# Performance work log

Measured on AMD Instinct MI355X. Metric: run time of the kernel, lower is better.

Reference implementation:

```python
import jax, jax.numpy as jnp
import numpy as np

N = 50000
E = 600000
H = 128   # hidden_channels (input to decoder)
O = 128   # output_channels (LSTM hidden size)
S = 8     # seq_len


def setup_inputs() -> dict:
    key = jax.random.key(0)
    ks = jax.random.split(key, 10)
    x = jax.random.normal(ks[0], (N, H), dtype=jnp.float32)
    c = jax.random.normal(ks[1], (N, H), dtype=jnp.float32)
    edge_index = jax.random.randint(ks[2], (2, E), 0, N, dtype=jnp.int64)
    # GCNConv weights (PyG: out = norm_agg(x @ W) + b)
    sc = lambda fan_in: 1.0 / np.sqrt(fan_in)
    Wh = jax.random.uniform(ks[3], (H, O), jnp.float32, -sc(H), sc(H))
    bh = jnp.zeros((O,), jnp.float32)
    Wc = jax.random.uniform(ks[4], (H, O), jnp.float32, -sc(H), sc(H))
    bc = jnp.zeros((O,), jnp.float32)
    # per-timestep cell convs: GCNConv(H + O, 4*O)
    Wcell = jax.random.uniform(ks[5], (S, H + O, 4 * O), jnp.float32, -sc(H + O), sc(H + O))
    bcell = jnp.zeros((S, 4 * O), jnp.float32)
    return {"x": x, "c": c, "edge_index": edge_index,
            "Wh": Wh, "bh": bh, "Wc": Wc, "bc": bc,
            "Wcell": Wcell, "bcell": bcell}


def _gcn(feat, W, b, src, dst, dinv):
    # PyG GCNConv with default add_self_loops=True, edge_weight=None:
    # out = D^{-1/2}(A+I)D^{-1/2} (feat @ W) + b
    xw = feat @ W                                   # [N, C_out]
    norm = (dinv[src] * dinv[dst])[:, None]         # [E, 1]
    agg = jax.ops.segment_sum(xw[src] * norm, dst, num_segments=N)
    agg = agg + (dinv * dinv)[:, None] * xw         # self-loop term
    return agg + b


def reference(x, c, edge_index, Wh, bh, Wc, bc, Wcell, bcell):
    src = edge_index[0]
    dst = edge_index[1]
    # degree (with self-loops, unit edge weights); computed on target index
    deg = jax.ops.segment_sum(jnp.ones((E,), jnp.float32), dst, num_segments=N) + 1.0
    dinv = 1.0 / jnp.sqrt(deg)

    h_cur = _gcn(x, Wh, bh, src, dst, dinv)
    c_cur = _gcn(c, Wc, bc, src, dst, dinv)

    def step(carry, params):
        h, cs = carry
        W, b = params
        combined = jnp.concatenate([x, h], axis=1)          # [N, H+O]
        cc = _gcn(combined, W, b, src, dst, dinv)           # [N, 4O]
        cc_f, cc_i, cc_o, cc_g = jnp.split(cc, 4, axis=1)
        f = jax.nn.sigmoid(cc_f)
        i = jax.nn.sigmoid(cc_i)
        o = jax.nn.sigmoid(cc_o)
        g = jnp.tanh(cc_g)
        c_next = f * cs + i * g
        h_next = o * jnp.tanh(c_next)
        return (h_next, c_next), h_next

    (h_fin, c_fin), hs = jax.lax.scan(step, (h_cur, c_cur), (Wcell, bcell))
    return hs, (h_fin, c_fin)  # hs: [S, N, O]
```

## Files before the change

### kernel.cpp

```cpp
#include <hip/hip_runtime.h>
#include <hip/hip_bf16.h>
#include <hip/hip_fp16.h>
#include <cstddef>


#define TPB 256

typedef __attribute__((ext_vector_type(8))) short bf16x8;
typedef __attribute__((ext_vector_type(4))) float f32x4;

__device__ __forceinline__ float sigf(float x) {
    return 1.0f / (1.0f + __expf(-x));
}
__device__ __forceinline__ float tanhfast(float x) {
    return 1.0f - 2.0f / (__expf(2.0f * x) + 1.0f);
}


__global__ void k_hist(const int* __restrict__ dst, int* __restrict__ counts, int E) {
    int stride = gridDim.x * TPB;
    for (int e = blockIdx.x * TPB + threadIdx.x; e < E; e += stride)
        atomicAdd(&counts[dst[e]], 1);
}

__global__ void k_scan_block(const int* __restrict__ counts, int* __restrict__ offsets,
                             int* __restrict__ sums, int N) {
    __shared__ int s[TPB];
    int tid = threadIdx.x;
    int gid = blockIdx.x * TPB + tid;
    int v = (gid < N) ? counts[gid] : 0;
    s[tid] = v;
    __syncthreads();
    for (int d = 1; d < TPB; d <<= 1) {
        int t = (tid >= d) ? s[tid - d] : 0;
        __syncthreads();
        s[tid] += t;
        __syncthreads();
    }
    if (gid < N) offsets[gid] = s[tid] - v;
    if (tid == TPB - 1) sums[blockIdx.x] = s[tid];
}

__global__ void k_scan_tops(int* __restrict__ sums, int nb) {
    __shared__ int s[TPB];
    int tid = threadIdx.x;
    int v = (tid < nb) ? sums[tid] : 0;
    s[tid] = v;
    __syncthreads();
    for (int d = 1; d < TPB; d <<= 1) {
        int t = (tid >= d) ? s[tid - d] : 0;
        __syncthreads();
        s[tid] += t;
        __syncthreads();
    }
    if (tid < nb) sums[tid] = s[tid] - v;
}

__global__ void k_scan_finish(const int* __restrict__ counts, int* __restrict__ offsets,
                              const int* __restrict__ sums, int* __restrict__ cursor,
                              float* __restrict__ dinv, int N, int E) {
    int gid = blockIdx.x * TPB + threadIdx.x;
    if (gid < N) {
        int off = offsets[gid] + sums[blockIdx.x];
        offsets[gid] = off;
        cursor[gid]  = off;
        dinv[gid]    = rsqrtf((float)(counts[gid] + 1));
    }
    if (gid == 0) offsets[N] = E;
}

__global__ void k_csr_scatter(const int* __restrict__ src, const int* __restrict__ dst,
                              const float* __restrict__ dinv, int* __restrict__ cursor,
                              int2* __restrict__ csr_sw, int E) {
    int stride = gridDim.x * TPB;
    for (int e = blockIdx.x * TPB + threadIdx.x; e < E; e += stride) {
        int d = dst[e], s = src[e];
        int pos = atomicAdd(&cursor[d], 1);
        int2 r;
        r.x = s;
        r.y = __float_as_int(dinv[s] * dinv[d]);
        csr_sw[pos] = r;
    }
}


__global__ void k_f32tof16_2(const float* __restrict__ a, const float* __restrict__ b,
                             __half* __restrict__ oa, __half* __restrict__ ob, int n4) {
    int stride = gridDim.x * TPB;
    for (int i = blockIdx.x * TPB + threadIdx.x; i < n4; i += stride) {
        float4 va = ((const float4*)a)[i];
        float4 vb = ((const float4*)b)[i];
        ((__half2*)oa)[2 * i]     = __floats2half2_rn(va.x, va.y);
        ((__half2*)oa)[2 * i + 1] = __floats2half2_rn(va.z, va.w);
        ((__half2*)ob)[2 * i]     = __floats2half2_rn(vb.x, vb.y);
        ((__half2*)ob)[2 * i + 1] = __floats2half2_rn(vb.z, vb.w);
    }
}


union HU { f32x4 v; __half2 h[4]; };

__global__ __launch_bounds__(TPB) void k_aggregate_h(
        const __half* __restrict__ feat, __hip_bfloat16* __restrict__ agg,
        const int* __restrict__ offsets, const int2* __restrict__ sw,
        const float* __restrict__ dinv, int N) {
    int wid = blockIdx.x * 4 + (threadIdx.x >> 6);
    int nw = gridDim.x * 4;
    int lane = threadIdx.x & 63;
    int g = lane >> 4, t = lane & 15;
    const f32x4* f4 = (const f32x4*)feat;

    for (int n0 = wid * 2; n0 < N; n0 += nw * 2) {
        int n1 = n0 + 1;
        bool has1 = (n1 < N);
        int b0 = offsets[n0], e0 = offsets[n0 + 1];
        int b1 = has1 ? offsets[n1] : 0;
        int e1 = has1 ? offsets[n1 + 1] : 0;
        int s0 = (e0 > b0) ? e0 - 1 : 0;
        int s1 = (e1 > b1) ? e1 - 1 : 0;
        int it0 = (e0 - b0 + 3) >> 2;
        int it1 = (e1 - b1 + 3) >> 2;
        int nit = it0 > it1 ? it0 : it1;

        float acc0[8], acc1[8];
        #pragma unroll
        for (int j = 0; j < 8; ++j) { acc0[j] = 0.f; acc1[j] = 0.f; }

        for (int i = 0; i < nit; ++i) {
            int kk0 = b0 + 4 * i + g;
            int kc0 = (kk0 < e0) ? kk0 : s0;
            int kk1 = b1 + 4 * i + g;
            int kc1 = (kk1 < e1) ? kk1 : s1;
            int2 v0 = sw[kc0];
            int2 v1 = sw[kc1];
            float w0 = (kk0 < e0) ? __int_as_float(v0.y) : 0.f;
            float w1 = (kk1 < e1) ? __int_as_float(v1.y) : 0.f;
            HU u0, u1;
            u0.v = f4[(size_t)v0.x * 16 + t];
            u1.v = f4[(size_t)v1.x * 16 + t];
            #pragma unroll
            for (int j = 0; j < 4; ++j) {
                float2 p0 = __half22float2(u0.h[j]);
                float2 p1 = __half22float2(u1.h[j]);
                acc0[2 * j]     = fmaf(w0, p0.x, acc0[2 * j]);
                acc0[2 * j + 1] = fmaf(w0, p0.y, acc0[2 * j + 1]);
                acc1[2 * j]     = fmaf(w1, p1.x, acc1[2 * j]);
                acc1[2 * j + 1] = fmaf(w1, p1.y, acc1[2 * j + 1]);
            }
        }
        #pragma unroll
        for (int j = 0; j < 8; ++j) {
            acc0[j] += __shfl_xor(acc0[j], 16);
            acc0[j] += __shfl_xor(acc0[j], 32);
            acc1[j] += __shfl_xor(acc1[j], 16);
            acc1[j] += __shfl_xor(acc1[j], 32);
        }
        if (g == 0) {
            {
                float di = dinv[n0];
                float w0 = di * di;
                HU u;
                u.v = f4[(size_t)n0 * 16 + t];
                union { f32x4 v; __hip_bfloat162 b2[4]; } o;
                #pragma unroll
                for (int j = 0; j < 4; ++j) {
                    float2 vv = __half22float2(u.h[j]);
                    o.b2[j].x = __float2bfloat16(fmaf(w0, vv.x, acc0[2 * j]));
                    o.b2[j].y = __float2bfloat16(fmaf(w0, vv.y, acc0[2 * j + 1]));
                }
                *(f32x4*)(agg + (size_t)n0 * 128 + t * 8) = o.v;
            }
            if (has1) {
                float di = dinv[n1];
                float w0 = di * di;
                HU u;
                u.v = f4[(size_t)n1 * 16 + t];
                union { f32x4 v; __hip_bfloat162 b2[4]; } o;
                #pragma unroll
                for (int j = 0; j < 4; ++j) {
                    float2 vv = __half22float2(u.h[j]);
                    o.b2[j].x = __float2bfloat16(fmaf(w0, vv.x, acc1[2 * j]));
                    o.b2[j].y = __float2bfloat16(fmaf(w0, vv.y, acc1[2 * j + 1]));
                }
                *(f32x4*)(agg + (size_t)n1 * 128 + t * 8) = o.v;
            }
        }
    }
}

__global__ __launch_bounds__(TPB) void k_aggregate_h2(
        const __half* __restrict__ fa, const __half* __restrict__ fb,
        __hip_bfloat16* __restrict__ aggA, __hip_bfloat16* __restrict__ aggB,
        const int* __restrict__ offsets, const int2* __restrict__ sw,
        const float* __restrict__ dinv, int N) {
    int wgid = blockIdx.x * 4 + (threadIdx.x >> 6);
    int nwaves = gridDim.x * 4;
    int lane = threadIdx.x & 63;
    int g = lane >> 4, t = lane & 15;
    const f32x4* fa4 = (const f32x4*)fa;
    const f32x4* fb4 = (const f32x4*)fb;

    for (int node = wgid; node < N; node += nwaves) {
        float accA[8], accB[8];
        #pragma unroll
        for (int j = 0; j < 8; ++j) { accA[j] = 0.f; accB[j] = 0.f; }

        int b = offsets[node], e = offsets[node + 1];
        for (int k = b; k < e; k += 4) {
            int kk = k + g;
            int kkc = (kk < e) ? kk : (e - 1);
            int2 sv = sw[kkc];
            float w = (kk < e) ? __int_as_float(sv.y) : 0.f;
            size_t ri = (size_t)sv.x * 16 + t;
            HU ua, ub;
            ua.v = fa4[ri];
            ub.v = fb4[ri];
            #pragma unroll
            for (int j = 0; j < 4; ++j) {
                float2 va = __half22float2(ua.h[j]);
                float2 vb = __half22float2(ub.h[j]);
                accA[2 * j]     = fmaf(w, va.x, accA[2 * j]);
                accA[2 * j + 1] = fmaf(w, va.y, accA[2 * j + 1]);
                accB[2 * j]     = fmaf(w, vb.x, accB[2 * j]);
                accB[2 * j + 1] = fmaf(w, vb.y, accB[2 * j + 1]);
            }
        }
        #pragma unroll
        for (int j = 0; j < 8; ++j) {
            accA[j] += __shfl_xor(accA[j], 16);
            accA[j] += __shfl_xor(accA[j], 32);
            accB[j] += __shfl_xor(accB[j], 16);
            accB[j] += __shfl_xor(accB[j], 32);
        }
        if (g == 0) {
            float di = dinv[node];
            float w0 = di * di;
            size_t ri = (size_t)node * 16 + t;
            HU ua, ub;
            ua.v = fa4[ri];
            ub.v = fb4[ri];
            union { f32x4 v; __hip_bfloat162 b2[4]; } oa, ob;
            #pragma unroll
            for (int j = 0; j < 4; ++j) {
                float2 va = __half22float2(ua.h[j]);
                float2 vb = __half22float2(ub.h[j]);
                oa.b2[j].x = __float2bfloat16(fmaf(w0, va.x, accA[2 * j]));
                oa.b2[j].y = __float2bfloat16(fmaf(w0, va.y, accA[2 * j + 1]));
                ob.b2[j].x = __float2bfloat16(fmaf(w0, vb.x, accB[2 * j]));
                ob.b2[j].y = __float2bfloat16(fmaf(w0, vb.y, accB[2 * j + 1]));
            }
            *(f32x4*)(aggA + (size_t)node * 128 + t * 8) = oa.v;
            *(f32x4*)(aggB + (size_t)node * 128 + t * 8) = ob.v;
        }
    }
}


__global__ void k_pack_w128_2(const float* __restrict__ Wh, const float* __restrict__ Wc,
                              __hip_bfloat16* __restrict__ WhP, __hip_bfloat16* __restrict__ WcP) {
    int gid = blockIdx.x * TPB + threadIdx.x;
    if (gid >= 32768) return;
    const float* W = (gid < 16384) ? Wh : Wc;
    __hip_bfloat16* Wp = (gid < 16384) ? WhP : WcP;
    int idx = gid & 16383;
    int j = idx & 7, lane = (idx >> 3) & 63, pblk = (idx >> 9) & 7, ks = idx >> 12;
    int k = ks * 32 + (lane >> 4) * 8 + j;
    int col = pblk * 16 + (lane & 15);
    Wp[idx] = __float2bfloat16(W[k * 128 + col]);
}

__global__ void k_pack_wcell(const float* __restrict__ W, __hip_bfloat16* __restrict__ Wp, int S) {
    int total = S * 131072;
    int stride = gridDim.x * TPB;
    for (int idx = blockIdx.x * TPB + threadIdx.x; idx < total; idx += stride) {
        int j = idx & 7, lane = (idx >> 3) & 63, pblk = (idx >> 9) & 31;
        int ks = (idx >> 14) & 7, s = idx >> 17;
        int p = pblk * 16 + (lane & 15);
        int jcol = p >> 2, gate = p & 3;
        int k = ks * 32 + (lane >> 4) * 8 + j;
        Wp[idx] = __float2bfloat16(W[(size_t)s * 131072 + k * 512 + gate * 128 + jcol]);
    }
}


__global__ __launch_bounds__(TPB) void k_gemm_t(
        const __hip_bfloat16* __restrict__ Ap,
        const __hip_bfloat16* __restrict__ featb,
        const float* __restrict__ bias, float* __restrict__ Cout,
        __half* __restrict__ outh, int N) {
    __shared__ __align__(16) short Bs[128 * 40];
    int tid = threadIdx.x;
    int wave = tid >> 6, lane = tid & 63;
    int w_p = wave >> 1, w_n = wave & 1;
    int n0 = blockIdx.x * 128;
    int quad = lane >> 4, m16 = lane & 15;
    f32x4 zero = {0.f, 0.f, 0.f, 0.f};
    f32x4 acc[4][4];
    #pragma unroll
    for (int t = 0; t < 4; ++t)
        #pragma unroll
        for (int g = 0; g < 4; ++g) acc[t][g] = zero;

    for (int ks = 0; ks < 4; ++ks) {
        int kbase = ks * 32;
        __syncthreads();
        #pragma unroll
        for (int it = 0; it < 2; ++it) {
            int lin = it * TPB + tid;
            int row = lin >> 2, seg = lin & 3;
            int node = n0 + row;
            f32x4 v = zero;
            if (node < N) v = *(const f32x4*)(featb + (size_t)node * 128 + kbase + seg * 8);
            *(f32x4*)&Bs[row * 40 + seg * 8] = v;
        }
        __syncthreads();
        bf16x8 a[4], b[4];
        #pragma unroll
        for (int t = 0; t < 4; ++t)
            a[t] = *(const bf16x8*)(Ap + (((size_t)ks * 8 + w_p * 4 + t) * 64 + lane) * 8);
        #pragma unroll
        for (int g = 0; g < 4; ++g)
            b[g] = *(const bf16x8*)&Bs[(w_n * 64 + g * 16 + m16) * 40 + quad * 8];
        #pragma unroll
        for (int t = 0; t < 4; ++t)
            #pragma unroll
            for (int g = 0; g < 4; ++g)
                acc[t][g] = __builtin_amdgcn_mfma_f32_16x16x32_bf16(a[t], b[g], acc[t][g], 0, 0, 0);
    }
    #pragma unroll
    for (int t = 0; t < 4; ++t) {
        int p = w_p * 64 + t * 16 + quad * 4;
        f32x4 bv = *(const f32x4*)(bias + p);
        #pragma unroll
        for (int g = 0; g < 4; ++g) {
            int nd = n0 + w_n * 64 + g * 16 + m16;
            if (nd < N) {
                f32x4 o = acc[t][g] + bv;
                if (Cout) *(f32x4*)(Cout + (size_t)nd * 128 + p) = o;
                if (outh) {
                    __half2 lo = __floats2half2_rn(o.x, o.y);
                    __half2 hi = __floats2half2_rn(o.z, o.w);
                    __half2* hp = (__half2*)(outh + (size_t)nd * 128 + p);
                    hp[0] = lo;
                    hp[1] = hi;
                }
            }
        }
    }
}


__global__ __launch_bounds__(TPB) void k_cell_t(
        const __hip_bfloat16* __restrict__ Ap,
        const __hip_bfloat16* __restrict__ axb, const __hip_bfloat16* __restrict__ ahb,
        const float* __restrict__ bias,
        float* __restrict__ cbuf, float* __restrict__ hout,
        __half* __restrict__ houth,
        float* __restrict__ hfin, int N) {
    __shared__ __align__(16) short Bs[8][128 * 40];
    int tid = threadIdx.x;
    int wave = tid >> 6, lane = tid & 63;
    int w_p = wave >> 1, w_n = wave & 1;
    int n0 = blockIdx.x * 128;
    int quad = lane >> 4, m16 = lane & 15;
    f32x4 zero = {0.f, 0.f, 0.f, 0.f};

    #pragma unroll
    for (int it = 0; it < 16; ++it) {
        int ks = it >> 1;
        int lin = ((it & 1) << 8) + tid;
        int row = lin >> 2, seg = lin & 3;
        const __hip_bfloat16* fsrc = (ks < 4) ? axb : ahb;
        int node = n0 + row;
        f32x4 v = zero;
        if (node < N) v = *(const f32x4*)(fsrc + (size_t)node * 128 + (ks & 3) * 32 + seg * 8);
        *(f32x4*)&Bs[ks][row * 40 + seg * 8] = v;
    }
    __syncthreads();

    for (int p0i = 0; p0i < 4; ++p0i) {
        f32x4 acc[4][4];
        #pragma unroll
        for (int t = 0; t < 4; ++t)
            #pragma unroll
            for (int g = 0; g < 4; ++g) acc[t][g] = zero;

        #pragma unroll
        for (int ks = 0; ks < 8; ++ks) {
            bf16x8 a[4], b[4];
            #pragma unroll
            for (int t = 0; t < 4; ++t)
                a[t] = *(const bf16x8*)(Ap + (((size_t)ks * 32 + p0i * 8 + w_p * 4 + t) * 64 + lane) * 8);
            #pragma unroll
            for (int g = 0; g < 4; ++g)
                b[g] = *(const bf16x8*)&Bs[ks][(w_n * 64 + g * 16 + m16) * 40 + quad * 8];
            #pragma unroll
            for (int t = 0; t < 4; ++t)
                #pragma unroll
                for (int g = 0; g < 4; ++g)
                    acc[t][g] = __builtin_amdgcn_mfma_f32_16x16x32_bf16(a[t], b[g], acc[t][g], 0, 0, 0);
        }

        #pragma unroll
        for (int t = 0; t < 4; ++t) {
            int p = p0i * 128 + w_p * 64 + t * 16 + quad * 4;
            int jcol = p >> 2;
            float bf = bias[jcol], bi = bias[128 + jcol], bo = bias[256 + jcol], bg = bias[384 + jcol];
            #pragma unroll
            for (int g = 0; g < 4; ++g) {
                int nd = n0 + w_n * 64 + g * 16 + m16;
                if (nd < N) {
                    float fv = sigf(acc[t][g].x + bf);
                    float iv = sigf(acc[t][g].y + bi);
                    float ov = sigf(acc[t][g].z + bo);
                    float gv = tanhfast(acc[t][g].w + bg);
                    size_t idx = (size_t)nd * 128 + jcol;
                    float cp = cbuf[idx];
                    float cn = fmaf(fv, cp, iv * gv);
                    cbuf[idx] = cn;
                    float hn = ov * tanhfast(cn);
                    hout[idx] = hn;
                    houth[idx] = __float2half(hn);
                    if (hfin) hfin[idx] = hn;
                }
            }
        }
    }
}


extern "C" void kernel_launch(void* const* d_in, const int* in_sizes, int n_in,
                              void* d_out, int out_size, void* d_ws, size_t ws_size,
                              hipStream_t stream) {
    const float* x  = (const float*)d_in[0];
    const float* c  = (const float*)d_in[1];
    const int*   ei = (const int*)d_in[2];
    const float* Wh = (const float*)d_in[3];
    const float* bh = (const float*)d_in[4];
    const float* Wc = (const float*)d_in[5];
    const float* bc = (const float*)d_in[6];
    const float* Wcell = (const float*)d_in[7];
    const float* bcell = (const float*)d_in[8];
    float* out = (float*)d_out;

    const int N = in_sizes[0] / 128;
    const int E = in_sizes[2] / 2;
    const int S = in_sizes[7] / (256 * 512);
    const int* srcp = ei;
    const int* dstp = ei + E;

    float* hs   = out;
    float* hfin = out + (size_t)S * N * 128;
    float* cbuf = hfin + (size_t)N * 128;

    char* w = (char*)d_ws;
    size_t off = 0;
    auto alloc = [&](size_t bytes) -> void* {
        void* p = w + off;
        off += (bytes + 255) & ~(size_t)255;
        return p;
    };
    int*   counts  = (int*)alloc((size_t)N * 4);
    int*   offsets = (int*)alloc((size_t)(N + 1) * 4);
    int*   cursor  = (int*)alloc((size_t)N * 4);
    int*   sums    = (int*)alloc(256 * 4);
    int2*  csr_sw  = (int2*)alloc((size_t)E * 8);
    float* dinv    = (float*)alloc((size_t)N * 4);
    __hip_bfloat16* axb = (__hip_bfloat16*)alloc((size_t)N * 128 * 2);
    __hip_bfloat16* acb = (__hip_bfloat16*)alloc((size_t)N * 128 * 2);
    __half* xh = (__half*)alloc((size_t)N * 128 * 2);
    __half* ch = (__half*)alloc((size_t)N * 128 * 2);
    __half* hh = (__half*)alloc((size_t)N * 128 * 2);
    __hip_bfloat16* WhP = (__hip_bfloat16*)alloc(16384 * 2);
    __hip_bfloat16* WcP = (__hip_bfloat16*)alloc(16384 * 2);
    __hip_bfloat16* WcellP = (__hip_bfloat16*)alloc((size_t)S * 131072 * 2);
    (void)ws_size; (void)n_in; (void)out_size;

    hipMemsetAsync(counts, 0, (size_t)N * 4, stream);
    int nb = (N + TPB - 1) / TPB;
    k_hist<<<1024, TPB, 0, stream>>>(dstp, counts, E);
    k_scan_block<<<nb, TPB, 0, stream>>>(counts, offsets, sums, N);
    k_scan_tops<<<1, TPB, 0, stream>>>(sums, nb);
    k_scan_finish<<<nb, TPB, 0, stream>>>(counts, offsets, sums, cursor, dinv, N, E);
    k_csr_scatter<<<1024, TPB, 0, stream>>>(srcp, dstp, dinv, cursor, csr_sw, E);

    k_pack_w128_2<<<128, TPB, 0, stream>>>(Wh, Wc, WhP, WcP);
    k_pack_wcell<<<1024, TPB, 0, stream>>>(Wcell, WcellP, S);

    int n4 = N * 128 / 4;
    k_f32tof16_2<<<1024, TPB, 0, stream>>>(x, c, xh, ch, n4);

    int ngt = (N + 127) / 128;
    k_aggregate_h2<<<2048, TPB, 0, stream>>>(xh, ch, axb, acb, offsets, csr_sw, dinv, N);
    k_gemm_t<<<ngt, TPB, 0, stream>>>(WhP, axb, bh, nullptr, hh, N);
    k_gemm_t<<<ngt, TPB, 0, stream>>>(WcP, acb, bc, cbuf, nullptr, N);

    for (int s = 0; s < S; ++s) {
        k_aggregate_h<<<2048, TPB, 0, stream>>>(hh, acb, offsets, csr_sw, dinv, N);
        k_cell_t<<<ngt, TPB, 0, stream>>>(
            WcellP + (size_t)s * 131072, axb, acb, bcell + (size_t)s * 512,
            cbuf, hs + (size_t)s * N * 128, hh, (s == S - 1) ? hfin : nullptr, N);
    }
}
```

Baseline: 1.283 ms.

## Sort nodes by degree for balanced aggregation; merge the two initial GEMMs

Builds a per-node permutation grouped by in-degree (64-bin counting sort) and has the aggregation kernels walk nodes in that order. In k_aggregate_h this pairs nodes of similar degree, so less work is wasted on the padded loop when the two nodes differ. It also merges the two initial GCN GEMM launches into one 2D grid. The risks are extra setup kernels and less locality in output writes and feature gathers, because neighbouring nodes in processing order are no longer contiguous in memory.

Measured after the change: 1.614 ms. 25.9% more time.

```diff
diff --git a/kernel.cpp b/kernel.cpp
--- a/kernel.cpp
+++ b/kernel.cpp
@@ -58,15 +58,42 @@
 
 __global__ void k_scan_finish(const int* __restrict__ counts, int* __restrict__ offsets,
                               const int* __restrict__ sums, int* __restrict__ cursor,
-                              float* __restrict__ dinv, int N, int E) {
+                              float* __restrict__ dinv, int* __restrict__ dh,
+                              int N, int E) {
     int gid = blockIdx.x * TPB + threadIdx.x;
     if (gid < N) {
         int off = offsets[gid] + sums[blockIdx.x];
         offsets[gid] = off;
         cursor[gid]  = off;
-        dinv[gid]    = rsqrtf((float)(counts[gid] + 1));
+        int cnt = counts[gid];
+        dinv[gid]    = rsqrtf((float)(cnt + 1));
+        atomicAdd(&dh[cnt < 63 ? cnt : 63], 1);
     }
     if (gid == 0) offsets[N] = E;
+}
+
+__global__ void k_bin_scan(const int* __restrict__ dh, int* __restrict__ dcur) {
+    __shared__ int s[64];
+    int t = threadIdx.x;
+    if (t < 64) s[t] = dh[t];
+    __syncthreads();
+    if (t == 0) {
+        int acc = 0;
+        for (int i = 0; i < 64; ++i) { int v = s[i]; s[i] = acc; acc += v; }
+    }
+    __syncthreads();
+    if (t < 64) dcur[t] = s[t];
+}
+
+__global__ void k_perm_scatter(const int* __restrict__ counts, int* __restrict__ dcur,
+                               int* __restrict__ perm, int N) {
+    int stride = gridDim.x * TPB;
+    for (int n = blockIdx.x * TPB + threadIdx.x; n < N; n += stride) {
+        int d = counts[n];
+        if (d > 63) d = 63;
+        int pos = atomicAdd(&dcur[d], 1);
+        perm[pos] = n;
+    }
 }
 
 __global__ void k_csr_scatter(const int* __restrict__ src, const int* __restrict__ dst,
@@ -103,16 +130,17 @@
 __global__ __launch_bounds__(TPB) void k_aggregate_h(
         const __half* __restrict__ feat, __hip_bfloat16* __restrict__ agg,
         const int* __restrict__ offsets, const int2* __restrict__ sw,
-        const float* __restrict__ dinv, int N) {
+        const float* __restrict__ dinv, const int* __restrict__ perm, int N) {
     int wid = blockIdx.x * 4 + (threadIdx.x >> 6);
     int nw = gridDim.x * 4;
     int lane = threadIdx.x & 63;
     int g = lane >> 4, t = lane & 15;
     const f32x4* f4 = (const f32x4*)feat;
 
-    for (int n0 = wid * 2; n0 < N; n0 += nw * 2) {
-        int n1 = n0 + 1;
-        bool has1 = (n1 < N);
+    for (int pi = wid; 2 * pi < N; pi += nw) {
+        int n0 = perm[2 * pi];
+        bool has1 = (2 * pi + 1 < N);
+        int n1 = has1 ? perm[2 * pi + 1] : n0;
         int b0 = offsets[n0], e0 = offsets[n0 + 1];
         int b1 = has1 ? offsets[n1] : 0;
         int e1 = has1 ? offsets[n1 + 1] : 0;
@@ -192,7 +220,7 @@
         const __half* __restrict__ fa, const __half* __restrict__ fb,
         __hip_bfloat16* __restrict__ aggA, __hip_bfloat16* __restrict__ aggB,
         const int* __restrict__ offsets, const int2* __restrict__ sw,
-        const float* __restrict__ dinv, int N) {
+        const float* __restrict__ dinv, const int* __restrict__ perm, int N) {
     int wgid = blockIdx.x * 4 + (threadIdx.x >> 6);
     int nwaves = gridDim.x * 4;
     int lane = threadIdx.x & 63;
@@ -200,7 +228,8 @@
     const f32x4* fa4 = (const f32x4*)fa;
     const f32x4* fb4 = (const f32x4*)fb;
 
-    for (int node = wgid; node < N; node += nwaves) {
+    for (int idx = wgid; idx < N; idx += nwaves) {
+        int node = perm[idx];
         float accA[8], accB[8];
         #pragma unroll
         for (int j = 0; j < 8; ++j) { accA[j] = 0.f; accB[j] = 0.f; }
@@ -283,11 +312,16 @@
 }
 
 
-__global__ __launch_bounds__(TPB) void k_gemm_t(
-        const __hip_bfloat16* __restrict__ Ap,
-        const __hip_bfloat16* __restrict__ featb,
-        const float* __restrict__ bias, float* __restrict__ Cout,
-        __half* __restrict__ outh, int N) {
+__global__ __launch_bounds__(TPB) void k_gemm_t2(
+        const __hip_bfloat16* __restrict__ WhP, const __hip_bfloat16* __restrict__ WcP,
+        const __hip_bfloat16* __restrict__ axb, const __hip_bfloat16* __restrict__ acb,
+        const float* __restrict__ bh, const float* __restrict__ bc,
+        float* __restrict__ cbuf, __half* __restrict__ hh, int N) {
+    const int which = blockIdx.y;
+    const __hip_bfloat16* Ap    = which ? WcP : WhP;
+    const __hip_bfloat16* featb = which ? acb : axb;
+    const float* bias           = which ? bc  : bh;
+
     __shared__ __align__(16) short Bs[128 * 40];
     int tid = threadIdx.x;
     int wave = tid >> 6, lane = tid & 63;
@@ -336,11 +370,12 @@
             int nd = n0 + w_n * 64 + g * 16 + m16;
             if (nd < N) {
                 f32x4 o = acc[t][g] + bv;
-                if (Cout) *(f32x4*)(Cout + (size_t)nd * 128 + p) = o;
-                if (outh) {
+                if (which) {
+                    *(f32x4*)(cbuf + (size_t)nd * 128 + p) = o;
+                } else {
                     __half2 lo = __floats2half2_rn(o.x, o.y);
                     __half2 hi = __floats2half2_rn(o.z, o.w);
-                    __half2* hp = (__half2*)(outh + (size_t)nd * 128 + p);
+                    __half2* hp = (__half2*)(hh + (size_t)nd * 128 + p);
                     hp[0] = lo;
                     hp[1] = hi;
                 }
@@ -464,6 +499,9 @@
     int*   offsets = (int*)alloc((size_t)(N + 1) * 4);
     int*   cursor  = (int*)alloc((size_t)N * 4);
     int*   sums    = (int*)alloc(256 * 4);
+    int*   dh      = (int*)alloc(64 * 4);
+    int*   dcur    = (int*)alloc(64 * 4);
+    int*   perm    = (int*)alloc((size_t)N * 4);
     int2*  csr_sw  = (int2*)alloc((size_t)E * 8);
     float* dinv    = (float*)alloc((size_t)N * 4);
     __hip_bfloat16* axb = (__hip_bfloat16*)alloc((size_t)N * 128 * 2);
@@ -477,11 +515,14 @@
     (void)ws_size; (void)n_in; (void)out_size;
 
     hipMemsetAsync(counts, 0, (size_t)N * 4, stream);
+    hipMemsetAsync(dh, 0, 64 * 4, stream);
     int nb = (N + TPB - 1) / TPB;
     k_hist<<<1024, TPB, 0, stream>>>(dstp, counts, E);
     k_scan_block<<<nb, TPB, 0, stream>>>(counts, offsets, sums, N);
     k_scan_tops<<<1, TPB, 0, stream>>>(sums, nb);
-    k_scan_finish<<<nb, TPB, 0, stream>>>(counts, offsets, sums, cursor, dinv, N, E);
+    k_scan_finish<<<nb, TPB, 0, stream>>>(counts, offsets, sums, cursor, dinv, dh, N, E);
+    k_bin_scan<<<1, 64, 0, stream>>>(dh, dcur);
+    k_perm_scatter<<<256, TPB, 0, stream>>>(counts, dcur, perm, N);
     k_csr_scatter<<<1024, TPB, 0, stream>>>(srcp, dstp, dinv, cursor, csr_sw, E);
 
     k_pack_w128_2<<<128, TPB, 0, stream>>>(Wh, Wc, WhP, WcP);
@@ -491,12 +532,11 @@
     k_f32tof16_2<<<1024, TPB, 0, stream>>>(x, c, xh, ch, n4);
 
     int ngt = (N + 127) / 128;
-    k_aggregate_h2<<<2048, TPB, 0, stream>>>(xh, ch, axb, acb, offsets, csr_sw, dinv, N);
-    k_gemm_t<<<ngt, TPB, 0, stream>>>(WhP, axb, bh, nullptr, hh, N);
-    k_gemm_t<<<ngt, TPB, 0, stream>>>(WcP, acb, bc, cbuf, nullptr, N);
+    k_aggregate_h2<<<2048, TPB, 0, stream>>>(xh, ch, axb, acb, offsets, csr_sw, dinv, perm, N);
+    k_gemm_t2<<<dim3(ngt, 2), TPB, 0, stream>>>(WhP, WcP, axb, acb, bh, bc, cbuf, hh, N);
 
     for (int s = 0; s < S; ++s) {
-        k_aggregate_h<<<2048, TPB, 0, stream>>>(hh, acb, offsets, csr_sw, dinv, N);
+        k_aggregate_h<<<2048, TPB, 0, stream>>>(hh, acb, offsets, csr_sw, dinv, perm, N);
         k_cell_t<<<ngt, TPB, 0, stream>>>(
             WcellP + (size_t)s * 131072, axb, acb, bcell + (size_t)s * 512,
             cbuf, hs + (size_t)s * N * 128, hh, (s == S - 1) ? hfin : nullptr, N);
```

## Halve cell-kernel node tile to 64 and merge the two initial GEMM launches

Applied to the files above, without the earlier changes.

The LSTM cell kernel now handles 64 nodes per block instead of 128. Each wave covers 2 gate tiles across all 64 nodes, so shared memory drops from 80KB to 40KB, the accumulator registers shrink, and the grid doubles to about 782 blocks. The aim is higher occupancy and better load balance across CUs. In exchange, each weight fragment is reused over fewer nodes, so reads of the packed weights from global/L2 double. Separately, the h and c initial GCN GEMMs are fused into one launch using blockIdx.y, which saves a launch.

Result: slower. 1.630 ms (+27.1%).

```diff
diff --git a/kernel.cpp b/kernel.cpp
--- a/kernel.cpp
+++ b/kernel.cpp
@@ -283,11 +283,16 @@
 }
 
 
-__global__ __launch_bounds__(TPB) void k_gemm_t(
-        const __hip_bfloat16* __restrict__ Ap,
-        const __hip_bfloat16* __restrict__ featb,
-        const float* __restrict__ bias, float* __restrict__ Cout,
-        __half* __restrict__ outh, int N) {
+__global__ __launch_bounds__(TPB) void k_gemm_t2(
+        const __hip_bfloat16* __restrict__ WhP, const __hip_bfloat16* __restrict__ WcP,
+        const __hip_bfloat16* __restrict__ axb, const __hip_bfloat16* __restrict__ acb,
+        const float* __restrict__ bh, const float* __restrict__ bc,
+        float* __restrict__ cbuf, __half* __restrict__ hh, int N) {
+    const int which = blockIdx.y;
+    const __hip_bfloat16* Ap    = which ? WcP : WhP;
+    const __hip_bfloat16* featb = which ? acb : axb;
+    const float* bias           = which ? bc  : bh;
+
     __shared__ __align__(16) short Bs[128 * 40];
     int tid = threadIdx.x;
     int wave = tid >> 6, lane = tid & 63;
@@ -336,11 +341,12 @@
             int nd = n0 + w_n * 64 + g * 16 + m16;
             if (nd < N) {
                 f32x4 o = acc[t][g] + bv;
-                if (Cout) *(f32x4*)(Cout + (size_t)nd * 128 + p) = o;
-                if (outh) {
+                if (which) {
+                    *(f32x4*)(cbuf + (size_t)nd * 128 + p) = o;
+                } else {
                     __half2 lo = __floats2half2_rn(o.x, o.y);
                     __half2 hi = __floats2half2_rn(o.z, o.w);
-                    __half2* hp = (__half2*)(outh + (size_t)nd * 128 + p);
+                    __half2* hp = (__half2*)(hh + (size_t)nd * 128 + p);
                     hp[0] = lo;
                     hp[1] = hi;
                 }
@@ -357,58 +363,57 @@
         float* __restrict__ cbuf, float* __restrict__ hout,
         __half* __restrict__ houth,
         float* __restrict__ hfin, int N) {
-    __shared__ __align__(16) short Bs[8][128 * 40];
+    __shared__ __align__(16) short Bs[8][64 * 40];
     int tid = threadIdx.x;
     int wave = tid >> 6, lane = tid & 63;
-    int w_p = wave >> 1, w_n = wave & 1;
-    int n0 = blockIdx.x * 128;
+    int n0 = blockIdx.x * 64;
     int quad = lane >> 4, m16 = lane & 15;
     f32x4 zero = {0.f, 0.f, 0.f, 0.f};
 
-    #pragma unroll
-    for (int it = 0; it < 16; ++it) {
-        int ks = it >> 1;
-        int lin = ((it & 1) << 8) + tid;
-        int row = lin >> 2, seg = lin & 3;
-        const __hip_bfloat16* fsrc = (ks < 4) ? axb : ahb;
+    {
+        int row = tid >> 2, seg = tid & 3;
         int node = n0 + row;
-        f32x4 v = zero;
-        if (node < N) v = *(const f32x4*)(fsrc + (size_t)node * 128 + (ks & 3) * 32 + seg * 8);
-        *(f32x4*)&Bs[ks][row * 40 + seg * 8] = v;
+        #pragma unroll
+        for (int ks = 0; ks < 8; ++ks) {
+            const __hip_bfloat16* fsrc = (ks < 4) ? axb : ahb;
+            f32x4 v = zero;
+            if (node < N) v = *(const f32x4*)(fsrc + (size_t)node * 128 + (ks & 3) * 32 + seg * 8);
+            *(f32x4*)&Bs[ks][row * 40 + seg * 8] = v;
+        }
     }
     __syncthreads();
 
     for (int p0i = 0; p0i < 4; ++p0i) {
-        f32x4 acc[4][4];
-        #pragma unroll
-        for (int t = 0; t < 4; ++t)
+        f32x4 acc[2][4];
+        #pragma unroll
+        for (int t = 0; t < 2; ++t)
             #pragma unroll
             for (int g = 0; g < 4; ++g) acc[t][g] = zero;
 
         #pragma unroll
         for (int ks = 0; ks < 8; ++ks) {
-            bf16x8 a[4], b[4];
-            #pragma unroll
-            for (int t = 0; t < 4; ++t)
-                a[t] = *(const bf16x8*)(Ap + (((size_t)ks * 32 + p0i * 8 + w_p * 4 + t) * 64 + lane) * 8);
+            bf16x8 a[2], b[4];
+            #pragma unroll
+            for (int t = 0; t < 2; ++t)
+                a[t] = *(const bf16x8*)(Ap + (((size_t)ks * 32 + p0i * 8 + wave * 2 + t) * 64 + lane) * 8);
             #pragma unroll
             for (int g = 0; g < 4; ++g)
-                b[g] = *(const bf16x8*)&Bs[ks][(w_n * 64 + g * 16 + m16) * 40 + quad * 8];
-            #pragma unroll
-            for (int t = 0; t < 4; ++t)
+                b[g] = *(const bf16x8*)&Bs[ks][(g * 16 + m16) * 40 + quad * 8];
+            #pragma unroll
+            for (int t = 0; t < 2; ++t)
                 #pragma unroll
                 for (int g = 0; g < 4; ++g)
                     acc[t][g] = __builtin_amdgcn_mfma_f32_16x16x32_bf16(a[t], b[g], acc[t][g], 0, 0, 0);
         }
 
         #pragma unroll
-        for (int t = 0; t < 4; ++t) {
-            int p = p0i * 128 + w_p * 64 + t * 16 + quad * 4;
+        for (int t = 0; t < 2; ++t) {
+            int p = p0i * 128 + (wave * 2 + t) * 16 + quad * 4;
             int jcol = p >> 2;
             float bf = bias[jcol], bi = bias[128 + jcol], bo = bias[256 + jcol], bg = bias[384 + jcol];
             #pragma unroll
             for (int g = 0; g < 4; ++g) {
-                int nd = n0 + w_n * 64 + g * 16 + m16;
+                int nd = n0 + g * 16 + m16;
                 if (nd < N) {
                     float fv = sigf(acc[t][g].x + bf);
                     float iv = sigf(acc[t][g].y + bi);
@@ -490,14 +495,14 @@
     int n4 = N * 128 / 4;
     k_f32tof16_2<<<1024, TPB, 0, stream>>>(x, c, xh, ch, n4);
 
-    int ngt = (N + 127) / 128;
+    int ngt  = (N + 127) / 128;
+    int ngc  = (N + 63) / 64;
     k_aggregate_h2<<<2048, TPB, 0, stream>>>(xh, ch, axb, acb, offsets, csr_sw, dinv, N);
-    k_gemm_t<<<ngt, TPB, 0, stream>>>(WhP, axb, bh, nullptr, hh, N);
-    k_gemm_t<<<ngt, TPB, 0, stream>>>(WcP, acb, bc, cbuf, nullptr, N);
+    k_gemm_t2<<<dim3(ngt, 2), TPB, 0, stream>>>(WhP, WcP, axb, acb, bh, bc, cbuf, hh, N);
 
     for (int s = 0; s < S; ++s) {
         k_aggregate_h<<<2048, TPB, 0, stream>>>(hh, acb, offsets, csr_sw, dinv, N);
-        k_cell_t<<<ngt, TPB, 0, stream>>>(
+        k_cell_t<<<ngc, TPB, 0, stream>>>(
             WcellP + (size_t)s * 131072, axb, acb, bcell + (size_t)s * 512,
             cbuf, hs + (size_t)s * N * 128, hh, (s == S - 1) ? hfin : nullptr, N);
     }
```
